# Kernel optimization log

Hardware: AMD Instinct MI355X
Metric: run time of the kernel (lower is better)

The kernel has to match this reference:

```python
import jax, jax.numpy as jnp
import numpy as np

B, S, C, H, D = 2, 2048, 1024, 16, 64  # hidden C must equal H*D (value is a reshape of key_states)


def setup_inputs() -> dict:
    key = jax.random.key(0)
    ks = jax.random.split(key, 7)
    query_states = jax.random.normal(ks[0], (B, S, C), dtype=jnp.float32)
    key_states = jax.random.normal(ks[1], (B, S, C), dtype=jnp.float32)
    attention_mask = jax.random.randint(ks[2], (B, 1, 1, S), 0, 2).astype(jnp.int32)
    Wq = jax.random.normal(ks[3], (C, H, D), dtype=jnp.float32) * 0.02
    bq = jnp.zeros((H, D), dtype=jnp.float32)
    Wk = jax.random.normal(ks[4], (C, H, D), dtype=jnp.float32) * 0.02
    bk = jnp.zeros((H, D), dtype=jnp.float32)
    return {
        "query_states": query_states,
        "key_states": key_states,
        "attention_mask": attention_mask,
        "Wq": Wq,
        "bq": bq,
        "Wk": Wk,
        "bk": bk,
    }


def reference(query_states, key_states, attention_mask, Wq, bq, Wk, bk):
    # EinsumDense 'abc,cde->abde' with bias on 'de'
    q = jnp.einsum("bsc,chd->bshd", query_states, Wq) + bq  # [B,S,H,D]
    k = jnp.einsum("bsc,chd->bshd", key_states, Wk) + bk    # [B,S,H,D]
    # value is just key_states reshaped into head layout (no projection!)
    v = key_states.reshape(k.shape)                          # [B,S,H,D]
    # scale query by 1/sqrt(dk)
    q = q * jax.lax.rsqrt(jnp.asarray(D, q.dtype))
    # 'aecd,abcd->acbe': a=batch, c=head, b=query pos, e=key pos
    scores = jnp.einsum("bkhd,bqhd->bhqk", k, q)             # [B,H,Sq,Sk]
    mask = (1.0 - attention_mask.astype(scores.dtype)) * -10000.0
    scores = scores + mask
    probs = jax.nn.softmax(scores, axis=-1)
    # dropout is identity at training=False (default)
    # 'acbe,aecd->abcd': weighted sum of values over key positions
    out = jnp.einsum("bhqk,bkhd->bqhd", probs, v)            # [B,S,H,D]
    return out
```

## Files before the change

### kernel.cpp

```cpp
#include <hip/hip_runtime.h>

#define BSZ 2
#define SEQ 2048
#define CH  1024
#define NH  16
#define HD  64
#define LOG2E 1.4426950408889634f
#define MASKC (-14426.950408889634f)

typedef short  bf16x8 __attribute__((ext_vector_type(8)));
typedef short  bf16x4 __attribute__((ext_vector_type(4)));
typedef float  f32x4  __attribute__((ext_vector_type(4)));

__device__ __forceinline__ short f2bf(float f) {
    union { float f; unsigned u; } v; v.f = f;
    unsigned r = v.u + 0x7FFFu + ((v.u >> 16) & 1u);
    return (short)(r >> 16);
}
__device__ __forceinline__ float exp2_hw(float x) {
#if __has_builtin(__builtin_amdgcn_exp2f)
    return __builtin_amdgcn_exp2f(x);
#else
    float r;
    asm volatile("v_exp_f32 %0, %1\n\ts_nop 1" : "=v"(r) : "v"(x));
    return r;
#endif
}

__device__ __forceinline__ bf16x4 pack4_rne(float p0, float p1, float p2, float p3) {
    unsigned lo, hi;
    asm("s_nop 1\n\t"
        "v_cvt_pk_bf16_f32 %0, %2, %3\n\t"
        "v_cvt_pk_bf16_f32 %1, %4, %5"
        : "=&v"(lo), "=&v"(hi)
        : "v"(p0), "v"(p1), "v"(p2), "v"(p3));
    union { unsigned u[2]; bf16x4 v; } r;
    r.u[0] = lo; r.u[1] = hi;
    return r.v;
}

#if __has_builtin(__builtin_amdgcn_mfma_f32_16x16x16bf16_1k)
__device__ __forceinline__ f32x4 mfma16x16x16(bf16x4 a, bf16x4 b, f32x4 c) {
    return __builtin_amdgcn_mfma_f32_16x16x16bf16_1k(a, b, c, 0, 0, 0);
}
#else
__device__ __forceinline__ f32x4 mfma16x16x16(bf16x4 a, bf16x4 b, f32x4 c) {
    f32x4 d;
    asm("v_mfma_f32_16x16x16_bf16 %0, %1, %2, %3"
        : "=v"(d) : "v"(a), "v"(b), "v"(c));
    return d;
}
#endif

__global__ __launch_bounds__(256) void prep(
    const float* __restrict__ query, const float* __restrict__ key,
    const float* __restrict__ Wq, const float* __restrict__ Wk,
    short* __restrict__ qc, short* __restrict__ kc,
    short* __restrict__ wtq, short* __restrict__ wtk,
    short* __restrict__ vtr)
{
    __shared__ float tile[64][65];
    const int bid = blockIdx.x;
    const int tid = threadIdx.x;

    if (bid < 4096) {
        const float* s = (bid < 2048) ? query : key;
        short*       d = (bid < 2048) ? qc : kc;
        long i = ((long)(bid & 2047) * 256 + tid) * 8;
        float4 v0 = *(const float4*)&s[i];
        float4 v1 = *(const float4*)&s[i + 4];
        bf16x8 o;
        o[0] = f2bf(v0.x); o[1] = f2bf(v0.y); o[2] = f2bf(v0.z); o[3] = f2bf(v0.w);
        o[4] = f2bf(v1.x); o[5] = f2bf(v1.y); o[6] = f2bf(v1.z); o[7] = f2bf(v1.w);
        *(bf16x8*)&d[i] = o;
        return;
    }

    const float* s; short* d;
    int r0, c0, srs, drs;
    if (bid < 4608) {
        int t = bid - 4096;
        s   = (t < 256) ? Wq : Wk;
        d   = (t < 256) ? wtq : wtk;
        t  &= 255;
        r0  = (t >> 4) * 64;
        c0  = (t & 15) * 64;
        srs = CH; drs = CH;
    } else {
        int t = bid - 4608;
        int z = t >> 5;
        int sy = t & 31;
        s   = key + (long)(z >> 4) * SEQ * CH + (long)(z & 15) * HD;
        d   = vtr + (long)z * HD * SEQ;
        r0  = sy * 64;
        c0  = 0;
        srs = CH; drs = SEQ;
    }

    const int r  = tid >> 2;
    const int c4 = (tid & 3) << 4;
    #pragma unroll
    for (int i = 0; i < 16; i += 4) {
        float4 v = *(const float4*)&s[(long)(r0 + r) * srs + c0 + c4 + i];
        tile[r][c4 + i + 0] = v.x;
        tile[r][c4 + i + 1] = v.y;
        tile[r][c4 + i + 2] = v.z;
        tile[r][c4 + i + 3] = v.w;
    }
    __syncthreads();
    bf16x8 o0, o1;
    #pragma unroll
    for (int i = 0; i < 8; i++) o0[i] = f2bf(tile[c4 + i][r]);
    #pragma unroll
    for (int i = 0; i < 8; i++) o1[i] = f2bf(tile[c4 + 8 + i][r]);
    *(bf16x8*)&d[(long)(c0 + r) * drs + r0 + c4 + 0] = o0;
    *(bf16x8*)&d[(long)(c0 + r) * drs + r0 + c4 + 8] = o1;
}

__global__ __launch_bounds__(256, 2) void proj_mfma(
    const short* __restrict__ Xq, const short* __restrict__ Xk,
    const short* __restrict__ Wtq, const short* __restrict__ Wtk,
    const float* __restrict__ bq_, const float* __restrict__ bk_,
    short* __restrict__ Yq, short* __restrict__ Yk)
{
    __shared__ short At[2][128 * 72];
    __shared__ short Bt[2][128 * 72];

    const int bid  = blockIdx.x;
    const int g    = bid >> 3, xcd = bid & 7;
    const int pair = ((g >> 3) << 3) | xcd;
    const int xt   = g & 7;
    const int yy   = pair >> 1;
    const int zz   = pair & 1;

    const short* X    = zz ? Xk  : Xq;
    const short* Wt   = zz ? Wtk : Wtq;
    const float* bias = zz ? bk_ : bq_;
    short*       Y    = zz ? Yk  : Yq;
    const float scale = zz ? 1.0f : (0.125f * LOG2E);

    const int tid  = threadIdx.x;
    const int lane = tid & 63, w = tid >> 6;
    const int quad = lane >> 4, t16 = lane & 15;
    const int m0 = yy * 128, n0 = xt * 128;
    const int srow = tid >> 1;
    const int shalf = (tid & 1) * 32;

    f32x4 acc[4][4];
    #pragma unroll
    for (int i = 0; i < 4; i++)
        #pragma unroll
        for (int j = 0; j < 4; j++)
            acc[i][j] = (f32x4){0.f, 0.f, 0.f, 0.f};

    const int M0 = (w >> 1) * 64, N0 = (w & 1) * 64;
    const int NIT = CH / 64;

    bf16x8 ar[4], br[4];
    #pragma unroll
    for (int c = 0; c < 4; c++) {
        ar[c] = *(const bf16x8*)&X [(long)(m0 + srow) * CH + shalf + 8 * c];
        br[c] = *(const bf16x8*)&Wt[(long)(n0 + srow) * CH + shalf + 8 * c];
    }
    #pragma unroll
    for (int c = 0; c < 4; c++) {
        *(bf16x8*)&At[0][srow * 72 + shalf + 8 * c] = ar[c];
        *(bf16x8*)&Bt[0][srow * 72 + shalf + 8 * c] = br[c];
    }
    #pragma unroll
    for (int c = 0; c < 4; c++) {
        ar[c] = *(const bf16x8*)&X [(long)(m0 + srow) * CH + 64 + shalf + 8 * c];
        br[c] = *(const bf16x8*)&Wt[(long)(n0 + srow) * CH + 64 + shalf + 8 * c];
    }
    __syncthreads();

    for (int it = 0; it < NIT; it++) {
        const int buf = it & 1;
        if (it + 1 < NIT) {
            #pragma unroll
            for (int c = 0; c < 4; c++) {
                *(bf16x8*)&At[buf ^ 1][srow * 72 + shalf + 8 * c] = ar[c];
                *(bf16x8*)&Bt[buf ^ 1][srow * 72 + shalf + 8 * c] = br[c];
            }
            if (it + 2 < NIT) {
                const long ko = (long)(it + 2) * 64;
                #pragma unroll
                for (int c = 0; c < 4; c++) {
                    ar[c] = *(const bf16x8*)&X [(long)(m0 + srow) * CH + ko + shalf + 8 * c];
                    br[c] = *(const bf16x8*)&Wt[(long)(n0 + srow) * CH + ko + shalf + 8 * c];
                }
            }
        }

        #pragma unroll
        for (int kk = 0; kk < 2; kk++) {
            bf16x8 af[4], bw[4];
            #pragma unroll
            for (int im = 0; im < 4; im++)
                af[im] = *(bf16x8*)&At[buf][(M0 + 16 * im + t16) * 72 + kk * 32 + quad * 8];
            #pragma unroll
            for (int jn = 0; jn < 4; jn++)
                bw[jn] = *(bf16x8*)&Bt[buf][(N0 + 16 * jn + t16) * 72 + kk * 32 + quad * 8];
            #pragma unroll
            for (int im = 0; im < 4; im++)
                #pragma unroll
                for (int jn = 0; jn < 4; jn++)
                    acc[im][jn] = __builtin_amdgcn_mfma_f32_16x16x32_bf16(
                        af[im], bw[jn], acc[im][jn], 0, 0, 0);
        }
        __syncthreads();
    }

    #pragma unroll
    for (int jn = 0; jn < 4; jn++) {
        float bs = bias[n0 + N0 + 16 * jn + t16];
        #pragma unroll
        for (int im = 0; im < 4; im++)
            #pragma unroll
            for (int reg = 0; reg < 4; reg++) {
                float y = (acc[im][jn][reg] + bs) * scale;
                Y[(long)(m0 + M0 + 16 * im + 4 * quad + reg) * (NH * HD)
                  + n0 + N0 + 16 * jn + t16] = f2bf(y);
            }
    }
}

__global__ __launch_bounds__(256, 2) void attn_mfma(
    const short* __restrict__ qp,
    const short* __restrict__ kp,
    const short* __restrict__ vt,
    const int*   __restrict__ amask,
    float* __restrict__ out)
{
    __shared__ short Kt[2][128 * 72];
    __shared__ short Vt[2][64 * 136];
    __shared__ float Msk[SEQ];

    const int bid = blockIdx.x;
    const int g   = bid >> 3, xcd = bid & 7;
    const int hb  = ((g >> 4) << 3) | xcd;
    const int qt  = g & 15;

    const int qt0 = qt * 128;
    const int h   = hb & 15;
    const int b   = hb >> 4;
    const int tid = threadIdx.x;
    const int lane = tid & 63, w = tid >> 6;
    const int quad = lane >> 4, t16 = lane & 15;

    {
        int4 a0 = *(const int4*)&amask[b * SEQ + tid * 8];
        int4 a1 = *(const int4*)&amask[b * SEQ + tid * 8 + 4];
        float4 f0 = {a0.x ? 0.f : MASKC, a0.y ? 0.f : MASKC,
                     a0.z ? 0.f : MASKC, a0.w ? 0.f : MASKC};
        float4 f1 = {a1.x ? 0.f : MASKC, a1.y ? 0.f : MASKC,
                     a1.z ? 0.f : MASKC, a1.w ? 0.f : MASKC};
        *(float4*)&Msk[tid * 8]     = f0;
        *(float4*)&Msk[tid * 8 + 4] = f1;
    }

    bf16x8 qf[2][2];
    #pragma unroll
    for (int qm = 0; qm < 2; qm++)
        #pragma unroll
        for (int ds = 0; ds < 2; ds++)
            qf[qm][ds] = *(const bf16x8*)&qp[
                (long)(b * SEQ + qt0 + w * 32 + qm * 16 + t16) * CH
                + h * HD + ds * 32 + quad * 8];

    f32x4 oa[4][2];
    float l_r[2];
    #pragma unroll
    for (int dt = 0; dt < 4; dt++)
        #pragma unroll
        for (int qm = 0; qm < 2; qm++)
            oa[dt][qm] = (f32x4){0.f, 0.f, 0.f, 0.f};
    l_r[0] = l_r[1] = 0.f;

    const int ksrow = tid >> 1;
    const int kscol = (tid & 1) * 32;
    const int vsrow = tid >> 2;
    const int vscol = (tid & 3) * 32;
    const long kbase = (long)(b * SEQ) * CH + h * HD;
    const long vbase = ((long)(b * NH + h) * HD) * SEQ;
    const int NIT = SEQ / 128;

    bf16x8 kr[4], vr[4];
    #pragma unroll
    for (int c = 0; c < 4; c++) {
        kr[c] = *(const bf16x8*)&kp[kbase + (long)ksrow * CH + kscol + 8 * c];
        vr[c] = *(const bf16x8*)&vt[vbase + (long)vsrow * SEQ + vscol + 8 * c];
    }
    #pragma unroll
    for (int c = 0; c < 4; c++) {
        *(bf16x8*)&Kt[0][ksrow * 72 + kscol + 8 * c] = kr[c];
        *(bf16x8*)&Vt[0][vsrow * 136 + vscol + 8 * c] = vr[c];
    }
    #pragma unroll
    for (int c = 0; c < 4; c++) {
        kr[c] = *(const bf16x8*)&kp[kbase + (long)(128 + ksrow) * CH + kscol + 8 * c];
        vr[c] = *(const bf16x8*)&vt[vbase + (long)vsrow * SEQ + 128 + vscol + 8 * c];
    }
    __syncthreads();

    for (int it = 0; it < NIT; it++) {
        const int buf = it & 1;
        const int kt0 = it * 128;

        if (it + 1 < NIT) {
            #pragma unroll
            for (int c = 0; c < 4; c++) {
                *(bf16x8*)&Kt[buf ^ 1][ksrow * 72 + kscol + 8 * c] = kr[c];
                *(bf16x8*)&Vt[buf ^ 1][vsrow * 136 + vscol + 8 * c] = vr[c];
            }
            if (it + 2 < NIT) {
                const int kn = kt0 + 256;
                #pragma unroll
                for (int c = 0; c < 4; c++) {
                    kr[c] = *(const bf16x8*)&kp[kbase + (long)(kn + ksrow) * CH + kscol + 8 * c];
                    vr[c] = *(const bf16x8*)&vt[vbase + (long)vsrow * SEQ + kn + vscol + 8 * c];
                }
            }
        }

        f32x4 sa[2][2][4];
        #pragma unroll
        for (int sub = 0; sub < 2; sub++) {
            const int ko = sub * 64;

            float4 mv4[4];
            #pragma unroll
            for (int jt = 0; jt < 4; jt++)
                mv4[jt] = *(const float4*)&Msk[kt0 + ko + jt * 16 + quad * 4];
            #pragma unroll
            for (int qm = 0; qm < 2; qm++)
                #pragma unroll
                for (int jt = 0; jt < 4; jt++)
                    sa[sub][qm][jt] = (f32x4){mv4[jt].x, mv4[jt].y, mv4[jt].z, mv4[jt].w};

            #pragma unroll
            for (int ds = 0; ds < 2; ds++) {
                bf16x8 kb[4];
                #pragma unroll
                for (int jt = 0; jt < 4; jt++)
                    kb[jt] = *(bf16x8*)&Kt[buf][(ko + jt * 16 + t16) * 72 + ds * 32 + quad * 8];
                __builtin_amdgcn_s_setprio(1);
                #pragma unroll
                for (int qm = 0; qm < 2; qm++)
                    #pragma unroll
                    for (int jt = 0; jt < 4; jt++)
                        sa[sub][qm][jt] = __builtin_amdgcn_mfma_f32_16x16x32_bf16(
                            kb[jt], qf[qm][ds], sa[sub][qm][jt], 0, 0, 0);
                __builtin_amdgcn_s_setprio(0);
            }
        }

        #pragma unroll
        for (int sub = 0; sub < 2; sub++) {
            const int ko = sub * 64;
            #pragma unroll
            for (int jt = 0; jt < 4; jt++) {
                bf16x4 pbq[2];
                #pragma unroll
                for (int qm = 0; qm < 2; qm++) {
                    float p0 = exp2_hw(sa[sub][qm][jt][0]);
                    float p1 = exp2_hw(sa[sub][qm][jt][1]);
                    float p2 = exp2_hw(sa[sub][qm][jt][2]);
                    float p3 = exp2_hw(sa[sub][qm][jt][3]);
                    l_r[qm] += (p0 + p1) + (p2 + p3);
                    pbq[qm] = pack4_rne(p0, p1, p2, p3);
                }
                bf16x4 va[4];
                #pragma unroll
                for (int dt = 0; dt < 4; dt++)
                    va[dt] = *(bf16x4*)&Vt[buf][(dt * 16 + t16) * 136 + ko + jt * 16 + quad * 4];
                __builtin_amdgcn_s_setprio(1);
                #pragma unroll
                for (int dt = 0; dt < 4; dt++)
                    #pragma unroll
                    for (int qm = 0; qm < 2; qm++)
                        oa[dt][qm] = mfma16x16x16(va[dt], pbq[qm], oa[dt][qm]);
                __builtin_amdgcn_s_setprio(0);
            }
        }
        __syncthreads();
    }

    #pragma unroll
    for (int qm = 0; qm < 2; qm++) {
        float l = l_r[qm];
        l += __shfl_xor(l, 16, 64);
        l += __shfl_xor(l, 32, 64);
        float inv = 1.0f / l;
        int q = qt0 + w * 32 + qm * 16 + t16;
        #pragma unroll
        for (int dt = 0; dt < 4; dt++) {
            f32x4 o = oa[dt][qm];
            float4 st = {o[0] * inv, o[1] * inv, o[2] * inv, o[3] * inv};
            *(float4*)&out[((long)(b * SEQ + q) * NH + h) * HD + dt * 16 + quad * 4] = st;
        }
    }
}

extern "C" void kernel_launch(void* const* d_in, const int* in_sizes, int n_in,
                              void* d_out, int out_size, void* d_ws, size_t ws_size,
                              hipStream_t stream) {
    const float* query = (const float*)d_in[0];
    const float* key   = (const float*)d_in[1];
    const int*   amask = (const int*)d_in[2];
    const float* Wq    = (const float*)d_in[3];
    const float* bq    = (const float*)d_in[4];
    const float* Wk    = (const float*)d_in[5];
    const float* bk    = (const float*)d_in[6];
    float* out = (float*)d_out;

    char* ws = (char*)d_ws;
    const long MB = 1024 * 1024;
    short* qc  = (short*)(ws + 0 * MB);
    short* kc  = (short*)(ws + 8 * MB);
    short* qp  = (short*)(ws + 16 * MB);
    short* kp  = (short*)(ws + 24 * MB);
    short* vtr = (short*)(ws + 32 * MB);
    short* wtq = (short*)(ws + 40 * MB);
    short* wtk = (short*)(ws + 42 * MB);

    prep<<<dim3(5632), 256, 0, stream>>>(query, key, Wq, Wk, qc, kc, wtq, wtk, vtr);

    proj_mfma<<<dim3(512), 256, 0, stream>>>(qc, kc, wtq, wtk, bq, bk, qp, kp);

    attn_mfma<<<dim3(512), 256, 0, stream>>>(qp, kp, vtr, amask, out);
}
```

Baseline: 174.3 us.

## Use direct global-to-LDS loads in projection GEMM and move V transpose there

The projection GEMM now stages its A and B tiles with `global_load_lds` 16-byte loads straight into shared memory. This replaces the old path of register prefetch followed by LDS stores, and drops the 72-element row padding because the direct loads need contiguous rows. The V transpose/convert work moves out of the prep kernel and into 1024 extra blocks of the projection kernel, reusing its shared buffer as the transpose tile, so the prep kernel launches fewer blocks. The unpadded 64-element row stride may cause LDS bank conflicts on the MFMA operand reads. The transpose tile also spills past the first buffer into the second, which relies on the two buffers being contiguous.

```diff
diff --git a/kernel.cpp b/kernel.cpp
--- a/kernel.cpp
+++ b/kernel.cpp
@@ -52,12 +52,22 @@
 }
 #endif
 
+__device__ __forceinline__ void gload16(const short* g, short* lbase, int lane) {
+#if __has_builtin(__builtin_amdgcn_global_load_lds)
+    (void)lane;
+    __builtin_amdgcn_global_load_lds(
+        (const __attribute__((address_space(1))) void*)g,
+        (__attribute__((address_space(3))) void*)lbase, 16, 0, 0);
+#else
+    *(bf16x8*)(lbase + lane * 8) = *(const bf16x8*)g;
+#endif
+}
+
 __global__ __launch_bounds__(256) void prep(
     const float* __restrict__ query, const float* __restrict__ key,
     const float* __restrict__ Wq, const float* __restrict__ Wk,
     short* __restrict__ qc, short* __restrict__ kc,
-    short* __restrict__ wtq, short* __restrict__ wtk,
-    short* __restrict__ vtr)
+    short* __restrict__ wtq, short* __restrict__ wtk)
 {
     __shared__ float tile[64][65];
     const int bid = blockIdx.x;
@@ -76,32 +86,18 @@
         return;
     }
 
-    const float* s; short* d;
-    int r0, c0, srs, drs;
-    if (bid < 4608) {
-        int t = bid - 4096;
-        s   = (t < 256) ? Wq : Wk;
-        d   = (t < 256) ? wtq : wtk;
-        t  &= 255;
-        r0  = (t >> 4) * 64;
-        c0  = (t & 15) * 64;
-        srs = CH; drs = CH;
-    } else {
-        int t = bid - 4608;
-        int z = t >> 5;
-        int sy = t & 31;
-        s   = key + (long)(z >> 4) * SEQ * CH + (long)(z & 15) * HD;
-        d   = vtr + (long)z * HD * SEQ;
-        r0  = sy * 64;
-        c0  = 0;
-        srs = CH; drs = SEQ;
-    }
+    int t = bid - 4096;
+    const float* s = (t < 256) ? Wq : Wk;
+    short*       d = (t < 256) ? wtq : wtk;
+    t &= 255;
+    const int r0 = (t >> 4) * 64;
+    const int c0 = (t & 15) * 64;
 
     const int r  = tid >> 2;
     const int c4 = (tid & 3) << 4;
     #pragma unroll
     for (int i = 0; i < 16; i += 4) {
-        float4 v = *(const float4*)&s[(long)(r0 + r) * srs + c0 + c4 + i];
+        float4 v = *(const float4*)&s[(long)(r0 + r) * CH + c0 + c4 + i];
         tile[r][c4 + i + 0] = v.x;
         tile[r][c4 + i + 1] = v.y;
         tile[r][c4 + i + 2] = v.z;
@@ -113,20 +109,52 @@
     for (int i = 0; i < 8; i++) o0[i] = f2bf(tile[c4 + i][r]);
     #pragma unroll
     for (int i = 0; i < 8; i++) o1[i] = f2bf(tile[c4 + 8 + i][r]);
-    *(bf16x8*)&d[(long)(c0 + r) * drs + r0 + c4 + 0] = o0;
-    *(bf16x8*)&d[(long)(c0 + r) * drs + r0 + c4 + 8] = o1;
+    *(bf16x8*)&d[(long)(c0 + r) * CH + r0 + c4 + 0] = o0;
+    *(bf16x8*)&d[(long)(c0 + r) * CH + r0 + c4 + 8] = o1;
 }
 
 __global__ __launch_bounds__(256, 2) void proj_mfma(
     const short* __restrict__ Xq, const short* __restrict__ Xk,
     const short* __restrict__ Wtq, const short* __restrict__ Wtk,
     const float* __restrict__ bq_, const float* __restrict__ bk_,
-    short* __restrict__ Yq, short* __restrict__ Yk)
+    short* __restrict__ Yq, short* __restrict__ Yk,
+    const float* __restrict__ key, short* __restrict__ vtr)
 {
-    __shared__ short At[2][128 * 72];
-    __shared__ short Bt[2][128 * 72];
-
-    const int bid  = blockIdx.x;
+    __shared__ short At[2][128 * 64];
+    __shared__ short Bt[2][128 * 64];
+
+    const int bid = blockIdx.x;
+    const int tid = threadIdx.x;
+
+    if (bid >= 512) {
+        float (*tile)[65] = (float (*)[65])&At[0][0];
+        int t = bid - 512;
+        int z = t >> 5;
+        int sy = t & 31;
+        const float* s = key + (long)(z >> 4) * SEQ * CH + (long)(z & 15) * HD;
+        short* d = vtr + (long)z * HD * SEQ;
+        const int r0 = sy * 64;
+        const int r  = tid >> 2;
+        const int c4 = (tid & 3) << 4;
+        #pragma unroll
+        for (int i = 0; i < 16; i += 4) {
+            float4 v = *(const float4*)&s[(long)(r0 + r) * CH + c4 + i];
+            tile[r][c4 + i + 0] = v.x;
+            tile[r][c4 + i + 1] = v.y;
+            tile[r][c4 + i + 2] = v.z;
+            tile[r][c4 + i + 3] = v.w;
+        }
+        __syncthreads();
+        bf16x8 o0, o1;
+        #pragma unroll
+        for (int i = 0; i < 8; i++) o0[i] = f2bf(tile[c4 + i][r]);
+        #pragma unroll
+        for (int i = 0; i < 8; i++) o1[i] = f2bf(tile[c4 + 8 + i][r]);
+        *(bf16x8*)&d[(long)r * SEQ + r0 + c4 + 0] = o0;
+        *(bf16x8*)&d[(long)r * SEQ + r0 + c4 + 8] = o1;
+        return;
+    }
+
     const int g    = bid >> 3, xcd = bid & 7;
     const int pair = ((g >> 3) << 3) | xcd;
     const int xt   = g & 7;
@@ -139,12 +167,9 @@
     short*       Y    = zz ? Yk  : Yq;
     const float scale = zz ? 1.0f : (0.125f * LOG2E);
 
-    const int tid  = threadIdx.x;
     const int lane = tid & 63, w = tid >> 6;
     const int quad = lane >> 4, t16 = lane & 15;
     const int m0 = yy * 128, n0 = xt * 128;
-    const int srow = tid >> 1;
-    const int shalf = (tid & 1) * 32;
 
     f32x4 acc[4][4];
     #pragma unroll
@@ -156,51 +181,36 @@
     const int M0 = (w >> 1) * 64, N0 = (w & 1) * 64;
     const int NIT = CH / 64;
 
-    bf16x8 ar[4], br[4];
-    #pragma unroll
-    for (int c = 0; c < 4; c++) {
-        ar[c] = *(const bf16x8*)&X [(long)(m0 + srow) * CH + shalf + 8 * c];
-        br[c] = *(const bf16x8*)&Wt[(long)(n0 + srow) * CH + shalf + 8 * c];
-    }
-    #pragma unroll
-    for (int c = 0; c < 4; c++) {
-        *(bf16x8*)&At[0][srow * 72 + shalf + 8 * c] = ar[c];
-        *(bf16x8*)&Bt[0][srow * 72 + shalf + 8 * c] = br[c];
-    }
-    #pragma unroll
-    for (int c = 0; c < 4; c++) {
-        ar[c] = *(const bf16x8*)&X [(long)(m0 + srow) * CH + 64 + shalf + 8 * c];
-        br[c] = *(const bf16x8*)&Wt[(long)(n0 + srow) * CH + 64 + shalf + 8 * c];
-    }
+    const int lrow = lane >> 3;
+    const int lcol = (lane & 7) * 8;
+    const short* ga = &X [(long)(m0 + w * 32 + lrow) * CH + lcol];
+    const short* gb = &Wt[(long)(n0 + w * 32 + lrow) * CH + lcol];
+
+    auto stage = [&](int buf, int ko) {
+        #pragma unroll
+        for (int j = 0; j < 4; j++) {
+            gload16(ga + (long)(j * 8) * CH + ko, &At[buf][(w * 32 + j * 8) * 64], lane);
+            gload16(gb + (long)(j * 8) * CH + ko, &Bt[buf][(w * 32 + j * 8) * 64], lane);
+        }
+    };
+
+    stage(0, 0);
     __syncthreads();
 
     for (int it = 0; it < NIT; it++) {
         const int buf = it & 1;
-        if (it + 1 < NIT) {
-            #pragma unroll
-            for (int c = 0; c < 4; c++) {
-                *(bf16x8*)&At[buf ^ 1][srow * 72 + shalf + 8 * c] = ar[c];
-                *(bf16x8*)&Bt[buf ^ 1][srow * 72 + shalf + 8 * c] = br[c];
-            }
-            if (it + 2 < NIT) {
-                const long ko = (long)(it + 2) * 64;
-                #pragma unroll
-                for (int c = 0; c < 4; c++) {
-                    ar[c] = *(const bf16x8*)&X [(long)(m0 + srow) * CH + ko + shalf + 8 * c];
-                    br[c] = *(const bf16x8*)&Wt[(long)(n0 + srow) * CH + ko + shalf + 8 * c];
-                }
-            }
-        }
+        if (it + 1 < NIT)
+            stage(buf ^ 1, (it + 1) * 64);
 
         #pragma unroll
         for (int kk = 0; kk < 2; kk++) {
             bf16x8 af[4], bw[4];
             #pragma unroll
             for (int im = 0; im < 4; im++)
-                af[im] = *(bf16x8*)&At[buf][(M0 + 16 * im + t16) * 72 + kk * 32 + quad * 8];
+                af[im] = *(bf16x8*)&At[buf][(M0 + 16 * im + t16) * 64 + kk * 32 + quad * 8];
             #pragma unroll
             for (int jn = 0; jn < 4; jn++)
-                bw[jn] = *(bf16x8*)&Bt[buf][(N0 + 16 * jn + t16) * 72 + kk * 32 + quad * 8];
+                bw[jn] = *(bf16x8*)&Bt[buf][(N0 + 16 * jn + t16) * 64 + kk * 32 + quad * 8];
             #pragma unroll
             for (int im = 0; im < 4; im++)
                 #pragma unroll
@@ -424,9 +434,10 @@
     short* wtq = (short*)(ws + 40 * MB);
     short* wtk = (short*)(ws + 42 * MB);
 
-    prep<<<dim3(5632), 256, 0, stream>>>(query, key, Wq, Wk, qc, kc, wtq, wtk, vtr);
-
-    proj_mfma<<<dim3(512), 256, 0, stream>>>(qc, kc, wtq, wtk, bq, bk, qp, kp);
+    prep<<<dim3(4608), 256, 0, stream>>>(query, key, Wq, Wk, qc, kc, wtq, wtk);
+
+    proj_mfma<<<dim3(1536), 256, 0, stream>>>(qc, kc, wtq, wtk, bq, bk, qp, kp,
+                                              key, vtr);
 
     attn_mfma<<<dim3(512), 256, 0, stream>>>(qp, kp, vtr, amask, out);
 }
```

After: 181.3 us. 4.0% more time.
